# Performance work log

Hardware: AMD Instinct MI355X
Metric: run time of the kernel (lower is better)

## Reference

```python
import jax, jax.numpy as jnp
import numpy as np

D_MODEL = 512
NUM_HEADS = 8
HEAD_DIM = D_MODEL // NUM_HEADS
MAX_REL = 2


def setup_inputs() -> dict:
    key = jax.random.key(0)
    ks = jax.random.split(key, 12)
    B, S = 2, 4096
    std = 1.0 / np.sqrt(D_MODEL)
    inp = {
        'q': jax.random.normal(ks[0], (B, S, D_MODEL), jnp.float32),
        'k': jax.random.normal(ks[1], (B, S, D_MODEL), jnp.float32),
        'v': jax.random.normal(ks[2], (B, S, D_MODEL), jnp.float32),
        'Wq': jax.random.normal(ks[3], (D_MODEL, D_MODEL), jnp.float32) * std,
        'bq': jnp.zeros((D_MODEL,), jnp.float32),
        'Wk': jax.random.normal(ks[4], (D_MODEL, D_MODEL), jnp.float32) * std,
        'bk': jnp.zeros((D_MODEL,), jnp.float32),
        'Wv': jax.random.normal(ks[5], (D_MODEL, D_MODEL), jnp.float32) * std,
        'bv': jnp.zeros((D_MODEL,), jnp.float32),
        'Wo': jax.random.normal(ks[6], (D_MODEL, D_MODEL), jnp.float32) * std,
        'bo': jnp.zeros((D_MODEL,), jnp.float32),
        'rel_pos': jax.random.normal(ks[7], (NUM_HEADS, 2 * MAX_REL + 1), jnp.float32),
    }
    return inp


def _rel_bias(rel_pos, seq_len):
    pos = jnp.arange(seq_len)
    rel = pos[None, :] - pos[:, None]              # [S,S]
    idx = jnp.clip(rel, -MAX_REL, MAX_REL) + MAX_REL
    return rel_pos[:, idx]                         # [H,S,S]


def reference(q, k, v, Wq, bq, Wk, bk, Wv, bv, Wo, bo, rel_pos):
    B, S, D = q.shape
    H, Hd = NUM_HEADS, HEAD_DIM
    # torch Linear: x @ W.T + b
    Q = (q @ Wq.T + bq).reshape(B, S, H, Hd).transpose(0, 2, 1, 3)  # [B,H,S,Hd]
    K = (k @ Wk.T + bk).reshape(B, S, H, Hd).transpose(0, 2, 1, 3)
    V = (v @ Wv.T + bv).reshape(B, S, H, Hd).transpose(0, 2, 1, 3)
    scores = jnp.einsum('bhqd,bhkd->bhqk', Q, K) / jnp.sqrt(jnp.float32(Hd))
    scores = scores + _rel_bias(rel_pos, S)[None]                  # [B,H,S,S]
    probs = jax.nn.softmax(scores, axis=-1)
    attn = jnp.einsum('bhqk,bhkd->bhqd', probs, V)                 # [B,H,S,Hd]
    attn = attn.transpose(0, 2, 1, 3).reshape(B, S, D)
    return attn @ Wo.T + bo
```

## Files before the change

kernel.cpp:

```cpp
#include <hip/hip_runtime.h>

typedef __bf16 bf16_t;
typedef __bf16 bf16x4 __attribute__((ext_vector_type(4)));
typedef __bf16 bf16x8 __attribute__((ext_vector_type(8)));
typedef float f32x4 __attribute__((ext_vector_type(4)));

#define MFMA16(a, b, c) __builtin_amdgcn_mfma_f32_16x16x32_bf16(a, b, c, 0, 0, 0)
#define LOG2E 1.4426950408889634f

#define GLL(g, l)                                                      \
  __builtin_amdgcn_global_load_lds(                                    \
      (const __attribute__((address_space(1))) void*)(g),              \
      (__attribute__((address_space(3))) void*)(l), 16, 0, 0)

static constexpr int NB = 2;
static constexpr int SEQ = 4096;
static constexpr int DM = 512;
static constexpr int NH = 8;
static constexpr int HD = 64;
static constexpr int M_ROWS = NB * SEQ;

__global__ __launch_bounds__(256) void cvt_w_kernel(
    const float* __restrict__ w0, const float* __restrict__ w1,
    const float* __restrict__ w2, const float* __restrict__ w3,
    bf16_t* __restrict__ out) {
  const float* src = (blockIdx.y == 0) ? w0 : (blockIdx.y == 1) ? w1
                   : (blockIdx.y == 2) ? w2 : w3;
  int i = (blockIdx.x * 256 + threadIdx.x) * 4;
  float4 v = *(const float4*)(src + i);
  bf16_t* o = out + blockIdx.y * (DM * DM) + i;
  o[0] = (bf16_t)v.x; o[1] = (bf16_t)v.y; o[2] = (bf16_t)v.z; o[3] = (bf16_t)v.w;
}

template <int XMODE, int TM>
__device__ __forceinline__ void gemm_body(
    const void* __restrict__ Xv, const bf16_t* __restrict__ Wm,
    const float* __restrict__ bias, void* __restrict__ Out,
    int omode, float scale) {
  constexpr int MB = TM / 32;
  __shared__ bf16_t Asm[TM * 32];
  __shared__ bf16_t Bsm[128 * 32];

  const int tid = threadIdx.x;
  const int w = tid >> 6;
  const int lane = tid & 63;
  const int quad = lane >> 4, l15 = lane & 15;
  const int m0 = blockIdx.x * TM;
  const int n0 = blockIdx.y * 128;
  const int moff = (w & 1) * (TM / 2);
  const int noff = (w >> 1) * 64;

  const float* Xf = (const float*)Xv;
  const bf16_t* Xb = (const bf16_t*)Xv;

  f32x4 acc[MB][4];
#pragma unroll
  for (int mb = 0; mb < MB; mb++)
#pragma unroll
    for (int nb = 0; nb < 4; nb++) { acc[mb][nb][0] = 0.f; acc[mb][nb][1] = 0.f; acc[mb][nb][2] = 0.f; acc[mb][nb][3] = 0.f; }

  for (int k0 = 0; k0 < DM; k0 += 32) {
    __syncthreads();
#pragma unroll
    for (int j = 0; j < 2; j++) {
      const int c = w * 64 + lane + j * 256;
      GLL(Wm + (size_t)(n0 + (c >> 2)) * DM + k0 + (c & 3) * 8,
          Bsm + (w * 64 + j * 256) * 8);
    }
    if (XMODE == 1) {
#pragma unroll
      for (int j = 0; j < TM * 32 / 2048; j++) {
        const int c = w * 64 + lane + j * 256;
        GLL(Xb + (size_t)(m0 + (c >> 2)) * DM + k0 + (c & 3) * 8,
            Asm + (w * 64 + j * 256) * 8);
      }
    } else {
      const int arow = tid >> 1;
      const int aseg = (tid & 1) * 16;
      const float* src = Xf + (size_t)(m0 + arow) * DM + k0 + aseg;
      float4 x0 = *(const float4*)(src);
      float4 x1 = *(const float4*)(src + 4);
      float4 x2 = *(const float4*)(src + 8);
      float4 x3 = *(const float4*)(src + 12);
      bf16x8 p0, p1;
      p0[0] = (bf16_t)x0.x; p0[1] = (bf16_t)x0.y; p0[2] = (bf16_t)x0.z; p0[3] = (bf16_t)x0.w;
      p0[4] = (bf16_t)x1.x; p0[5] = (bf16_t)x1.y; p0[6] = (bf16_t)x1.z; p0[7] = (bf16_t)x1.w;
      p1[0] = (bf16_t)x2.x; p1[1] = (bf16_t)x2.y; p1[2] = (bf16_t)x2.z; p1[3] = (bf16_t)x2.w;
      p1[4] = (bf16_t)x3.x; p1[5] = (bf16_t)x3.y; p1[6] = (bf16_t)x3.z; p1[7] = (bf16_t)x3.w;
      *(bf16x8*)&Asm[arow * 32 + aseg] = p0;
      *(bf16x8*)&Asm[arow * 32 + aseg + 8] = p1;
    }
    __syncthreads();

    bf16x8 bfr[4];
#pragma unroll
    for (int nb = 0; nb < 4; nb++)
      bfr[nb] = *(const bf16x8*)&Bsm[(noff + nb * 16 + l15) * 32 + 8 * quad];
#pragma unroll
    for (int mb = 0; mb < MB; mb++) {
      bf16x8 a = *(const bf16x8*)&Asm[(moff + mb * 16 + l15) * 32 + 8 * quad];
#pragma unroll
      for (int nb = 0; nb < 4; nb++) acc[mb][nb] = MFMA16(a, bfr[nb], acc[mb][nb]);
    }
  }

#pragma unroll
  for (int nb = 0; nb < 4; nb++) {
    const int n = n0 + noff + nb * 16 + l15;
    const float bn = bias[n];
    const int h = n >> 6, dd = n & 63;
#pragma unroll
    for (int mb = 0; mb < MB; mb++) {
      const int mbase = m0 + moff + mb * 16 + quad * 4;
      const int bb = mbase >> 12, s = mbase & 4095;
      if (omode == 0) {
#pragma unroll
        for (int r = 0; r < 4; r++) {
          const float val = (acc[mb][nb][r] + bn) * scale;
          ((bf16_t*)Out)[(size_t)((bb * NH + h) * SEQ + s + r) * HD + dd] = (bf16_t)val;
        }
      } else if (omode == 1) {
        bf16x4 pk;
#pragma unroll
        for (int r = 0; r < 4; r++) pk[r] = (bf16_t)(acc[mb][nb][r] + bn);
        *(bf16x4*)&((bf16_t*)Out)[(((size_t)(bb * NH + h) * HD + dd) << 12) + s] = pk;
      } else {
#pragma unroll
        for (int r = 0; r < 4; r++)
          ((float*)Out)[(size_t)(mbase + r) * DM + n] = acc[mb][nb][r] + bn;
      }
    }
  }
}

__global__ __launch_bounds__(256, 3) void qkv_kernel(
    const float* __restrict__ q, const float* __restrict__ k,
    const float* __restrict__ v, const bf16_t* __restrict__ Wall,
    const float* __restrict__ bq, const float* __restrict__ bk,
    const float* __restrict__ bv, bf16_t* __restrict__ Qb,
    bf16_t* __restrict__ Kb, bf16_t* __restrict__ Vb, float qscale) {
  const int z = blockIdx.z;
  const float* X = (z == 0) ? q : (z == 1) ? k : v;
  const float* bias = (z == 0) ? bq : (z == 1) ? bk : bv;
  bf16_t* Out = (z == 0) ? Qb : (z == 1) ? Kb : Vb;
  gemm_body<0, 128>(X, Wall + (size_t)z * DM * DM, bias, Out,
                    (z == 2) ? 1 : 0, (z == 0) ? qscale : 1.0f);
}

__global__ __launch_bounds__(256, 3) void oproj_kernel(
    const bf16_t* __restrict__ X, const bf16_t* __restrict__ Wm,
    const float* __restrict__ bias, float* __restrict__ Out) {
  gemm_body<1, 64>(X, Wm, bias, Out, 2, 1.0f);
}

__global__ __launch_bounds__(256, 2) void attn_kernel(
    const bf16_t* __restrict__ Qb, const bf16_t* __restrict__ Kb,
    const bf16_t* __restrict__ Vb, const float* __restrict__ rel_pos,
    bf16_t* __restrict__ attn_out) {
  __shared__ bf16_t Kt[64 * 64];
  __shared__ bf16_t Vt[64 * 64];
  __shared__ bf16_t Pt[4][32 * 72];

  const int w = threadIdx.x >> 6;
  const int lane = threadIdx.x & 63;
  const int quad = lane >> 4, l15 = lane & 15;
  const int bh = blockIdx.y;
  const int b = bh >> 3, h = bh & 7;
  const int qlo = blockIdx.x * 128 + w * 32;

  const float rb0 = rel_pos[h * 5 + 0] * LOG2E;
  const float rb1 = rel_pos[h * 5 + 1] * LOG2E;
  const float rb2 = rel_pos[h * 5 + 2] * LOG2E;
  const float rb3 = rel_pos[h * 5 + 3] * LOG2E;
  const float rb4 = rel_pos[h * 5 + 4] * LOG2E;

  bf16x8 qf[2][2];
#pragma unroll
  for (int mb = 0; mb < 2; mb++)
#pragma unroll
    for (int kd = 0; kd < 2; kd++)
      qf[mb][kd] = *(const bf16x8*)(Qb + (size_t)(bh * SEQ + qlo + mb * 16 + l15) * HD + kd * 32 + 8 * quad);

  f32x4 o[2][4];
#pragma unroll
  for (int mb = 0; mb < 2; mb++)
#pragma unroll
    for (int db = 0; db < 4; db++) { o[mb][db][0] = 0.f; o[mb][db][1] = 0.f; o[mb][db][2] = 0.f; o[mb][db][3] = 0.f; }
  f32x4 l4[2];
  l4[0][0] = 0.f; l4[0][1] = 0.f; l4[0][2] = 0.f; l4[0][3] = 0.f;
  l4[1][0] = 0.f; l4[1][1] = 0.f; l4[1][2] = 0.f; l4[1][3] = 0.f;

  bf16x8 ones;
#pragma unroll
  for (int i = 0; i < 8; i++) ones[i] = (bf16_t)1.0f;

  const int srow = (w << 4) + (lane >> 3);
  const int scol = (((lane & 7) ^ (lane >> 3)) << 3);
  const bf16_t* kg0 = Kb + ((size_t)(bh * SEQ + srow) << 6) + scol;
  const bf16_t* kg1 = kg0 + (8 << 6);
  const bf16_t* vg0 = Vb + ((size_t)(bh * HD + srow) << 12) + scol;
  const bf16_t* vg1 = vg0 + (8 << 12);
  bf16_t* kl0 = Kt + (w << 10);
  bf16_t* kl1 = kl0 + 512;
  bf16_t* vl0 = Vt + (w << 10);
  bf16_t* vl1 = vl0 + 512;

  const int swz = l15 & 7;
  const bf16_t* kf0 = Kt + (l15 << 6) + (((quad    ) ^ swz) << 3);
  const bf16_t* kf1 = Kt + (l15 << 6) + (((quad + 4) ^ swz) << 3);
  const bf16_t* vf0 = Vt + (l15 << 6) + (((quad    ) ^ swz) << 3);
  const bf16_t* vf1 = Vt + (l15 << 6) + (((quad + 4) ^ swz) << 3);

  for (int t = 0; t < 64; t++) {
    const int kk0 = t * 64;
    __syncthreads();
    GLL(kg0 + (t << 12), kl0);
    GLL(kg1 + (t << 12), kl1);
    GLL(vg0 + (t << 6), vl0);
    GLL(vg1 + (t << 6), vl1);
    __syncthreads();

    float cini;
    bool nearband = false;
    if (kk0 >= qlo + 33) {
      cini = rb4 - 16.0f;
    } else if (kk0 + 63 <= qlo - 2) {
      cini = rb0 - 16.0f;
    } else {
      cini = -16.0f;
      nearband = true;
    }

    f32x4 s[2][4];
#pragma unroll
    for (int mb = 0; mb < 2; mb++)
#pragma unroll
      for (int kb = 0; kb < 4; kb++) { s[mb][kb][0] = cini; s[mb][kb][1] = cini; s[mb][kb][2] = cini; s[mb][kb][3] = cini; }
#pragma unroll
    for (int kb = 0; kb < 4; kb++) {
      bf16x8 kA0 = *(const bf16x8*)(kf0 + (kb << 10));
      bf16x8 kA1 = *(const bf16x8*)(kf1 + (kb << 10));
      s[0][kb] = MFMA16(kA0, qf[0][0], s[0][kb]);
      s[0][kb] = MFMA16(kA1, qf[0][1], s[0][kb]);
      s[1][kb] = MFMA16(kA0, qf[1][0], s[1][kb]);
      s[1][kb] = MFMA16(kA1, qf[1][1], s[1][kb]);
    }

    if (nearband) {
#pragma unroll
      for (int mb = 0; mb < 2; mb++) {
        const int qg = qlo + mb * 16 + l15;
#pragma unroll
        for (int kb = 0; kb < 4; kb++)
#pragma unroll
          for (int r = 0; r < 4; r++) {
            int dl = kk0 + kb * 16 + quad * 4 + r - qg;
            float bias = dl <= -2 ? rb0
                       : (dl >= 2 ? rb4
                       : (dl == -1 ? rb1 : (dl == 0 ? rb2 : rb3)));
            s[mb][kb][r] += bias;
          }
      }
    }

#pragma unroll
    for (int mb = 0; mb < 2; mb++) {
      bf16_t* Pr = &Pt[w][(mb * 16 + l15) * 72];
#pragma unroll
      for (int kb = 0; kb < 4; kb++) {
        bf16x4 pk;
#pragma unroll
        for (int r = 0; r < 4; r++)
          pk[r] = (bf16_t)__builtin_amdgcn_exp2f(s[mb][kb][r]);
        *(bf16x4*)&Pr[kb * 16 + quad * 4] = pk;
      }
    }

    bf16x8 pf[2][2];
#pragma unroll
    for (int mb = 0; mb < 2; mb++)
#pragma unroll
      for (int kc = 0; kc < 2; kc++)
        pf[mb][kc] = *(const bf16x8*)&Pt[w][(mb * 16 + l15) * 72 + kc * 32 + quad * 8];

    l4[0] = MFMA16(ones, pf[0][0], l4[0]);
    l4[0] = MFMA16(ones, pf[0][1], l4[0]);
    l4[1] = MFMA16(ones, pf[1][0], l4[1]);
    l4[1] = MFMA16(ones, pf[1][1], l4[1]);

#pragma unroll
    for (int db = 0; db < 4; db++) {
      bf16x8 vA0 = *(const bf16x8*)(vf0 + (db << 10));
      bf16x8 vA1 = *(const bf16x8*)(vf1 + (db << 10));
      o[0][db] = MFMA16(vA0, pf[0][0], o[0][db]);
      o[0][db] = MFMA16(vA1, pf[0][1], o[0][db]);
      o[1][db] = MFMA16(vA0, pf[1][0], o[1][db]);
      o[1][db] = MFMA16(vA1, pf[1][1], o[1][db]);
    }
  }

#pragma unroll
  for (int mb = 0; mb < 2; mb++) {
    const float inv = 1.0f / l4[mb][0];
    const int qg = qlo + mb * 16 + l15;
#pragma unroll
    for (int db = 0; db < 4; db++) {
      bf16x4 pk;
#pragma unroll
      for (int r = 0; r < 4; r++) pk[r] = (bf16_t)(o[mb][db][r] * inv);
      *(bf16x4*)(attn_out + (size_t)(b * SEQ + qg) * DM + h * HD + db * 16 + quad * 4) = pk;
    }
  }
}

extern "C" void kernel_launch(void* const* d_in, const int* in_sizes, int n_in,
                              void* d_out, int out_size, void* d_ws, size_t ws_size,
                              hipStream_t stream) {
  const float* q   = (const float*)d_in[0];
  const float* k   = (const float*)d_in[1];
  const float* v   = (const float*)d_in[2];
  const float* Wq  = (const float*)d_in[3];
  const float* bq  = (const float*)d_in[4];
  const float* Wk  = (const float*)d_in[5];
  const float* bk  = (const float*)d_in[6];
  const float* Wv  = (const float*)d_in[7];
  const float* bv  = (const float*)d_in[8];
  const float* Wo  = (const float*)d_in[9];
  const float* bo  = (const float*)d_in[10];
  const float* rel = (const float*)d_in[11];

  char* ws = (char*)d_ws;
  bf16_t* Wbf  = (bf16_t*)ws;
  bf16_t* Qbuf = (bf16_t*)(ws + (size_t)(2  << 20));
  bf16_t* Kbuf = (bf16_t*)(ws + (size_t)(10 << 20));
  bf16_t* Vbuf = (bf16_t*)(ws + (size_t)(18 << 20));
  bf16_t* Abuf = (bf16_t*)(ws + (size_t)(26 << 20));

  cvt_w_kernel<<<dim3(256, 4), 256, 0, stream>>>(Wq, Wk, Wv, Wo, Wbf);

  const float qscale = LOG2E / 8.0f;
  qkv_kernel<<<dim3(64, 4, 3), 256, 0, stream>>>(
      q, k, v, Wbf, bq, bk, bv, Qbuf, Kbuf, Vbuf, qscale);

  attn_kernel<<<dim3(32, 16), 256, 0, stream>>>(Qbuf, Kbuf, Vbuf, rel, Abuf);

  oproj_kernel<<<dim3(128, 4), 256, 0, stream>>>(Abuf, Wbf + 3 * DM * DM, bo, (float*)d_out);
}
```

Measured before the change: 241.3 us.

## Split attention keys across waves with LDS reduction; widen GEMM K-step to 64

The attention kernel now has each block own 64 queries, and each of its four waves handles a different 32-key slice. K and V fragments are loaded straight from global memory into registers, so the shared-memory staging and the per-iteration block barriers go away. Partial outputs and row sums are combined at the end through an LDS tree reduction, and the grid doubles to keep the block count up. The projection GEMMs switch to 64-wide K tiles with XOR-swizzled LDS to halve barrier count and avoid bank conflicts, at the cost of more LDS and uncoalesced direct global fragment loads in attention.

```diff
diff --git a/kernel.cpp b/kernel.cpp
--- a/kernel.cpp
+++ b/kernel.cpp
@@ -7,6 +7,7 @@
 
 #define MFMA16(a, b, c) __builtin_amdgcn_mfma_f32_16x16x32_bf16(a, b, c, 0, 0, 0)
 #define LOG2E 1.4426950408889634f
+#define SHIFT 16.0f
 
 #define GLL(g, l)                                                      \
   __builtin_amdgcn_global_load_lds(                                    \
@@ -38,69 +39,70 @@
     const float* __restrict__ bias, void* __restrict__ Out,
     int omode, float scale) {
   constexpr int MB = TM / 32;
-  __shared__ bf16_t Asm[TM * 32];
-  __shared__ bf16_t Bsm[128 * 32];
+  __shared__ bf16_t Asm[TM * 64];
+  __shared__ bf16_t Bsm[128 * 64];
 
   const int tid = threadIdx.x;
   const int w = tid >> 6;
   const int lane = tid & 63;
   const int quad = lane >> 4, l15 = lane & 15;
+  const int l8 = lane >> 3;
+  const int swcol = ((lane & 7) ^ l8) * 8;
   const int m0 = blockIdx.x * TM;
   const int n0 = blockIdx.y * 128;
   const int moff = (w & 1) * (TM / 2);
   const int noff = (w >> 1) * 64;
 
-  const float* Xf = (const float*)Xv;
-  const bf16_t* Xb = (const bf16_t*)Xv;
-
   f32x4 acc[MB][4];
 #pragma unroll
   for (int mb = 0; mb < MB; mb++)
 #pragma unroll
     for (int nb = 0; nb < 4; nb++) { acc[mb][nb][0] = 0.f; acc[mb][nb][1] = 0.f; acc[mb][nb][2] = 0.f; acc[mb][nb][3] = 0.f; }
 
-  for (int k0 = 0; k0 < DM; k0 += 32) {
+  for (int k0 = 0; k0 < DM; k0 += 64) {
     __syncthreads();
 #pragma unroll
-    for (int j = 0; j < 2; j++) {
-      const int c = w * 64 + lane + j * 256;
-      GLL(Wm + (size_t)(n0 + (c >> 2)) * DM + k0 + (c & 3) * 8,
-          Bsm + (w * 64 + j * 256) * 8);
+    for (int j = 0; j < 4; j++) {
+      const int row = j * 32 + w * 8 + l8;
+      GLL(Wm + (size_t)(n0 + row) * DM + k0 + swcol, Bsm + (j * 256 + w * 64) * 8);
     }
     if (XMODE == 1) {
 #pragma unroll
-      for (int j = 0; j < TM * 32 / 2048; j++) {
-        const int c = w * 64 + lane + j * 256;
-        GLL(Xb + (size_t)(m0 + (c >> 2)) * DM + k0 + (c & 3) * 8,
-            Asm + (w * 64 + j * 256) * 8);
+      for (int j = 0; j < TM / 32; j++) {
+        const int row = j * 32 + w * 8 + l8;
+        GLL((const bf16_t*)Xv + (size_t)(m0 + row) * DM + k0 + swcol,
+            Asm + (j * 256 + w * 64) * 8);
       }
     } else {
       const int arow = tid >> 1;
-      const int aseg = (tid & 1) * 16;
-      const float* src = Xf + (size_t)(m0 + arow) * DM + k0 + aseg;
-      float4 x0 = *(const float4*)(src);
-      float4 x1 = *(const float4*)(src + 4);
-      float4 x2 = *(const float4*)(src + 8);
-      float4 x3 = *(const float4*)(src + 12);
-      bf16x8 p0, p1;
-      p0[0] = (bf16_t)x0.x; p0[1] = (bf16_t)x0.y; p0[2] = (bf16_t)x0.z; p0[3] = (bf16_t)x0.w;
-      p0[4] = (bf16_t)x1.x; p0[5] = (bf16_t)x1.y; p0[6] = (bf16_t)x1.z; p0[7] = (bf16_t)x1.w;
-      p1[0] = (bf16_t)x2.x; p1[1] = (bf16_t)x2.y; p1[2] = (bf16_t)x2.z; p1[3] = (bf16_t)x2.w;
-      p1[4] = (bf16_t)x3.x; p1[5] = (bf16_t)x3.y; p1[6] = (bf16_t)x3.z; p1[7] = (bf16_t)x3.w;
-      *(bf16x8*)&Asm[arow * 32 + aseg] = p0;
-      *(bf16x8*)&Asm[arow * 32 + aseg + 8] = p1;
+      const int ahalf = (tid & 1) * 32;
+      const float* src = (const float*)Xv + (size_t)(m0 + arow) * DM + k0 + ahalf;
+      const int chb = (tid & 1) * 4;
+#pragma unroll
+      for (int i = 0; i < 4; i++) {
+        float4 lo = *(const float4*)(src + i * 8);
+        float4 hi = *(const float4*)(src + i * 8 + 4);
+        bf16x8 pk;
+        pk[0] = (bf16_t)lo.x; pk[1] = (bf16_t)lo.y; pk[2] = (bf16_t)lo.z; pk[3] = (bf16_t)lo.w;
+        pk[4] = (bf16_t)hi.x; pk[5] = (bf16_t)hi.y; pk[6] = (bf16_t)hi.z; pk[7] = (bf16_t)hi.w;
+        *(bf16x8*)&Asm[arow * 64 + (((chb + i) ^ (arow & 7)) * 8)] = pk;
+      }
     }
     __syncthreads();
 
-    bf16x8 bfr[4];
-#pragma unroll
-    for (int nb = 0; nb < 4; nb++)
-      bfr[nb] = *(const bf16x8*)&Bsm[(noff + nb * 16 + l15) * 32 + 8 * quad];
-#pragma unroll
-    for (int mb = 0; mb < MB; mb++) {
-      bf16x8 a = *(const bf16x8*)&Asm[(moff + mb * 16 + l15) * 32 + 8 * quad];
-#pragma unroll
-      for (int nb = 0; nb < 4; nb++) acc[mb][nb] = MFMA16(a, bfr[nb], acc[mb][nb]);
+#pragma unroll
+    for (int kd = 0; kd < 2; kd++) {
+      const int fch = ((kd * 4 + quad) ^ (l15 & 7)) * 8;
+      bf16x8 bfr[4];
+#pragma unroll
+      for (int nb = 0; nb < 4; nb++)
+        bfr[nb] = *(const bf16x8*)&Bsm[(noff + nb * 16 + l15) * 64 + fch];
+#pragma unroll
+      for (int mb = 0; mb < MB; mb++) {
+        bf16x8 a = *(const bf16x8*)&Asm[(moff + mb * 16 + l15) * 64 + fch];
+#pragma unroll
+        for (int nb = 0; nb < 4; nb++) acc[mb][nb] = MFMA16(a, bfr[nb], acc[mb][nb]);
+      }
     }
   }
 
@@ -157,16 +159,19 @@
     const bf16_t* __restrict__ Qb, const bf16_t* __restrict__ Kb,
     const bf16_t* __restrict__ Vb, const float* __restrict__ rel_pos,
     bf16_t* __restrict__ attn_out) {
-  __shared__ bf16_t Kt[64 * 64];
-  __shared__ bf16_t Vt[64 * 64];
-  __shared__ bf16_t Pt[4][32 * 72];
-
-  const int w = threadIdx.x >> 6;
-  const int lane = threadIdx.x & 63;
+  __shared__ char smem[34816];
+  const int tid = threadIdx.x;
+  const int w = tid >> 6;
+  const int lane = tid & 63;
   const int quad = lane >> 4, l15 = lane & 15;
   const int bh = blockIdx.y;
   const int b = bh >> 3, h = bh & 7;
-  const int qlo = blockIdx.x * 128 + w * 32;
+  const int qlo = blockIdx.x * 64;
+
+  bf16_t* Pw = (bf16_t*)smem + w * (64 * 40);
+  float* redA = (float*)smem;
+  float* redB = redA + 4096;
+  float* redL = redB + 4096;
 
   const float rb0 = rel_pos[h * 5 + 0] * LOG2E;
   const float rb1 = rel_pos[h * 5 + 1] * LOG2E;
@@ -174,141 +179,178 @@
   const float rb3 = rel_pos[h * 5 + 3] * LOG2E;
   const float rb4 = rel_pos[h * 5 + 4] * LOG2E;
 
-  bf16x8 qf[2][2];
-#pragma unroll
-  for (int mb = 0; mb < 2; mb++)
+  bf16x8 qf[4][2];
+#pragma unroll
+  for (int qb = 0; qb < 4; qb++)
 #pragma unroll
     for (int kd = 0; kd < 2; kd++)
-      qf[mb][kd] = *(const bf16x8*)(Qb + (size_t)(bh * SEQ + qlo + mb * 16 + l15) * HD + kd * 32 + 8 * quad);
-
-  f32x4 o[2][4];
-#pragma unroll
-  for (int mb = 0; mb < 2; mb++)
-#pragma unroll
-    for (int db = 0; db < 4; db++) { o[mb][db][0] = 0.f; o[mb][db][1] = 0.f; o[mb][db][2] = 0.f; o[mb][db][3] = 0.f; }
-  f32x4 l4[2];
-  l4[0][0] = 0.f; l4[0][1] = 0.f; l4[0][2] = 0.f; l4[0][3] = 0.f;
-  l4[1][0] = 0.f; l4[1][1] = 0.f; l4[1][2] = 0.f; l4[1][3] = 0.f;
+      qf[qb][kd] = *(const bf16x8*)(Qb + (size_t)(bh * SEQ + qlo + qb * 16 + l15) * HD + kd * 32 + 8 * quad);
+
+  f32x4 o[4][4];
+#pragma unroll
+  for (int db = 0; db < 4; db++)
+#pragma unroll
+    for (int qb = 0; qb < 4; qb++) { o[db][qb][0] = 0.f; o[db][qb][1] = 0.f; o[db][qb][2] = 0.f; o[db][qb][3] = 0.f; }
+  f32x4 l4[4];
+#pragma unroll
+  for (int qb = 0; qb < 4; qb++) { l4[qb][0] = 0.f; l4[qb][1] = 0.f; l4[qb][2] = 0.f; l4[qb][3] = 0.f; }
 
   bf16x8 ones;
 #pragma unroll
   for (int i = 0; i < 8; i++) ones[i] = (bf16_t)1.0f;
 
-  const int srow = (w << 4) + (lane >> 3);
-  const int scol = (((lane & 7) ^ (lane >> 3)) << 3);
-  const bf16_t* kg0 = Kb + ((size_t)(bh * SEQ + srow) << 6) + scol;
-  const bf16_t* kg1 = kg0 + (8 << 6);
-  const bf16_t* vg0 = Vb + ((size_t)(bh * HD + srow) << 12) + scol;
-  const bf16_t* vg1 = vg0 + (8 << 12);
-  bf16_t* kl0 = Kt + (w << 10);
-  bf16_t* kl1 = kl0 + 512;
-  bf16_t* vl0 = Vt + (w << 10);
-  bf16_t* vl1 = vl0 + 512;
-
-  const int swz = l15 & 7;
-  const bf16_t* kf0 = Kt + (l15 << 6) + (((quad    ) ^ swz) << 3);
-  const bf16_t* kf1 = Kt + (l15 << 6) + (((quad + 4) ^ swz) << 3);
-  const bf16_t* vf0 = Vt + (l15 << 6) + (((quad    ) ^ swz) << 3);
-  const bf16_t* vf1 = Vt + (l15 << 6) + (((quad + 4) ^ swz) << 3);
-
-  for (int t = 0; t < 64; t++) {
-    const int kk0 = t * 64;
-    __syncthreads();
-    GLL(kg0 + (t << 12), kl0);
-    GLL(kg1 + (t << 12), kl1);
-    GLL(vg0 + (t << 6), vl0);
-    GLL(vg1 + (t << 6), vl1);
-    __syncthreads();
+  const bf16_t* Kbase = Kb + (size_t)bh * SEQ * HD;
+  const bf16_t* Vbase = Vb + (((size_t)bh * HD) << 12);
+
+  for (int t = 0; t < 32; t++) {
+    const int kk0 = t * 128 + w * 32;
+
+    bf16x8 kA[2][2];
+#pragma unroll
+    for (int kkb = 0; kkb < 2; kkb++)
+#pragma unroll
+      for (int kd = 0; kd < 2; kd++)
+        kA[kkb][kd] = *(const bf16x8*)(Kbase + (size_t)(kk0 + kkb * 16 + l15) * HD + kd * 32 + quad * 8);
+    bf16x8 vA[4];
+#pragma unroll
+    for (int db = 0; db < 4; db++)
+      vA[db] = *(const bf16x8*)(Vbase + (((size_t)(db * 16 + l15)) << 12) + kk0 + quad * 8);
 
     float cini;
     bool nearband = false;
-    if (kk0 >= qlo + 33) {
-      cini = rb4 - 16.0f;
-    } else if (kk0 + 63 <= qlo - 2) {
-      cini = rb0 - 16.0f;
+    if (kk0 >= qlo + 65) {
+      cini = rb4 - SHIFT;
+    } else if (kk0 + 33 <= qlo) {
+      cini = rb0 - SHIFT;
     } else {
-      cini = -16.0f;
+      cini = -SHIFT;
       nearband = true;
     }
 
     f32x4 s[2][4];
 #pragma unroll
-    for (int mb = 0; mb < 2; mb++)
-#pragma unroll
-      for (int kb = 0; kb < 4; kb++) { s[mb][kb][0] = cini; s[mb][kb][1] = cini; s[mb][kb][2] = cini; s[mb][kb][3] = cini; }
-#pragma unroll
-    for (int kb = 0; kb < 4; kb++) {
-      bf16x8 kA0 = *(const bf16x8*)(kf0 + (kb << 10));
-      bf16x8 kA1 = *(const bf16x8*)(kf1 + (kb << 10));
-      s[0][kb] = MFMA16(kA0, qf[0][0], s[0][kb]);
-      s[0][kb] = MFMA16(kA1, qf[0][1], s[0][kb]);
-      s[1][kb] = MFMA16(kA0, qf[1][0], s[1][kb]);
-      s[1][kb] = MFMA16(kA1, qf[1][1], s[1][kb]);
-    }
+    for (int kkb = 0; kkb < 2; kkb++)
+#pragma unroll
+      for (int qb = 0; qb < 4; qb++) { s[kkb][qb][0] = cini; s[kkb][qb][1] = cini; s[kkb][qb][2] = cini; s[kkb][qb][3] = cini; }
+#pragma unroll
+    for (int kkb = 0; kkb < 2; kkb++)
+#pragma unroll
+      for (int qb = 0; qb < 4; qb++) {
+        s[kkb][qb] = MFMA16(kA[kkb][0], qf[qb][0], s[kkb][qb]);
+        s[kkb][qb] = MFMA16(kA[kkb][1], qf[qb][1], s[kkb][qb]);
+      }
 
     if (nearband) {
 #pragma unroll
-      for (int mb = 0; mb < 2; mb++) {
-        const int qg = qlo + mb * 16 + l15;
-#pragma unroll
-        for (int kb = 0; kb < 4; kb++)
+      for (int kkb = 0; kkb < 2; kkb++)
+#pragma unroll
+        for (int qb = 0; qb < 4; qb++) {
+          const int qg = qlo + qb * 16 + l15;
 #pragma unroll
           for (int r = 0; r < 4; r++) {
-            int dl = kk0 + kb * 16 + quad * 4 + r - qg;
+            int dl = kk0 + kkb * 16 + quad * 4 + r - qg;
             float bias = dl <= -2 ? rb0
                        : (dl >= 2 ? rb4
                        : (dl == -1 ? rb1 : (dl == 0 ? rb2 : rb3)));
-            s[mb][kb][r] += bias;
+            s[kkb][qb][r] += bias;
           }
-      }
-    }
-
-#pragma unroll
-    for (int mb = 0; mb < 2; mb++) {
-      bf16_t* Pr = &Pt[w][(mb * 16 + l15) * 72];
-#pragma unroll
-      for (int kb = 0; kb < 4; kb++) {
+        }
+    }
+
+#pragma unroll
+    for (int qb = 0; qb < 4; qb++) {
+      bf16_t* Pr = &Pw[(qb * 16 + l15) * 40];
+#pragma unroll
+      for (int kkb = 0; kkb < 2; kkb++) {
         bf16x4 pk;
 #pragma unroll
         for (int r = 0; r < 4; r++)
-          pk[r] = (bf16_t)__builtin_amdgcn_exp2f(s[mb][kb][r]);
-        *(bf16x4*)&Pr[kb * 16 + quad * 4] = pk;
-      }
-    }
-
-    bf16x8 pf[2][2];
-#pragma unroll
-    for (int mb = 0; mb < 2; mb++)
-#pragma unroll
-      for (int kc = 0; kc < 2; kc++)
-        pf[mb][kc] = *(const bf16x8*)&Pt[w][(mb * 16 + l15) * 72 + kc * 32 + quad * 8];
-
-    l4[0] = MFMA16(ones, pf[0][0], l4[0]);
-    l4[0] = MFMA16(ones, pf[0][1], l4[0]);
-    l4[1] = MFMA16(ones, pf[1][0], l4[1]);
-    l4[1] = MFMA16(ones, pf[1][1], l4[1]);
-
-#pragma unroll
-    for (int db = 0; db < 4; db++) {
-      bf16x8 vA0 = *(const bf16x8*)(vf0 + (db << 10));
-      bf16x8 vA1 = *(const bf16x8*)(vf1 + (db << 10));
-      o[0][db] = MFMA16(vA0, pf[0][0], o[0][db]);
-      o[0][db] = MFMA16(vA1, pf[0][1], o[0][db]);
-      o[1][db] = MFMA16(vA0, pf[1][0], o[1][db]);
-      o[1][db] = MFMA16(vA1, pf[1][1], o[1][db]);
-    }
-  }
-
-#pragma unroll
-  for (int mb = 0; mb < 2; mb++) {
-    const float inv = 1.0f / l4[mb][0];
-    const int qg = qlo + mb * 16 + l15;
-#pragma unroll
-    for (int db = 0; db < 4; db++) {
-      bf16x4 pk;
-#pragma unroll
-      for (int r = 0; r < 4; r++) pk[r] = (bf16_t)(o[mb][db][r] * inv);
-      *(bf16x4*)(attn_out + (size_t)(b * SEQ + qg) * DM + h * HD + db * 16 + quad * 4) = pk;
+          pk[r] = (bf16_t)__builtin_amdgcn_exp2f(s[kkb][qb][r]);
+        *(bf16x4*)&Pr[kkb * 16 + quad * 4] = pk;
+      }
+    }
+
+    bf16x8 pf[4];
+#pragma unroll
+    for (int qb = 0; qb < 4; qb++)
+      pf[qb] = *(const bf16x8*)&Pw[(qb * 16 + l15) * 40 + quad * 8];
+#pragma unroll
+    for (int qb = 0; qb < 4; qb++) l4[qb] = MFMA16(ones, pf[qb], l4[qb]);
+#pragma unroll
+    for (int db = 0; db < 4; db++)
+#pragma unroll
+      for (int qb = 0; qb < 4; qb++)
+        o[db][qb] = MFMA16(vA[db], pf[qb], o[db][qb]);
+  }
+
+  __syncthreads();
+  if (w == 2) {
+#pragma unroll
+    for (int db = 0; db < 4; db++)
+#pragma unroll
+      for (int qb = 0; qb < 4; qb++)
+        *(f32x4*)&redA[((db * 4 + qb) * 64 + lane) * 4] = o[db][qb];
+  }
+  if (w == 3) {
+#pragma unroll
+    for (int db = 0; db < 4; db++)
+#pragma unroll
+      for (int qb = 0; qb < 4; qb++)
+        *(f32x4*)&redB[((db * 4 + qb) * 64 + lane) * 4] = o[db][qb];
+  }
+  if (quad == 0) {
+#pragma unroll
+    for (int qb = 0; qb < 4; qb++) redL[w * 64 + qb * 16 + l15] = l4[qb][0];
+  }
+  __syncthreads();
+  if (w == 0) {
+#pragma unroll
+    for (int db = 0; db < 4; db++)
+#pragma unroll
+      for (int qb = 0; qb < 4; qb++) {
+        f32x4 tv = *(const f32x4*)&redA[((db * 4 + qb) * 64 + lane) * 4];
+        o[db][qb][0] += tv[0]; o[db][qb][1] += tv[1]; o[db][qb][2] += tv[2]; o[db][qb][3] += tv[3];
+      }
+  }
+  if (w == 1) {
+#pragma unroll
+    for (int db = 0; db < 4; db++)
+#pragma unroll
+      for (int qb = 0; qb < 4; qb++) {
+        f32x4 tv = *(const f32x4*)&redB[((db * 4 + qb) * 64 + lane) * 4];
+        o[db][qb][0] += tv[0]; o[db][qb][1] += tv[1]; o[db][qb][2] += tv[2]; o[db][qb][3] += tv[3];
+      }
+  }
+  __syncthreads();
+  if (w == 1) {
+#pragma unroll
+    for (int db = 0; db < 4; db++)
+#pragma unroll
+      for (int qb = 0; qb < 4; qb++)
+        *(f32x4*)&redA[((db * 4 + qb) * 64 + lane) * 4] = o[db][qb];
+  }
+  __syncthreads();
+  if (w == 0) {
+#pragma unroll
+    for (int db = 0; db < 4; db++)
+#pragma unroll
+      for (int qb = 0; qb < 4; qb++) {
+        f32x4 tv = *(const f32x4*)&redA[((db * 4 + qb) * 64 + lane) * 4];
+        o[db][qb][0] += tv[0]; o[db][qb][1] += tv[1]; o[db][qb][2] += tv[2]; o[db][qb][3] += tv[3];
+      }
+#pragma unroll
+    for (int qb = 0; qb < 4; qb++) {
+      const int q16 = qb * 16 + l15;
+      const float lt = redL[q16] + redL[64 + q16] + redL[128 + q16] + redL[192 + q16];
+      const float inv = 1.0f / lt;
+      const int qg = qlo + q16;
+#pragma unroll
+      for (int db = 0; db < 4; db++) {
+        bf16x4 pk;
+#pragma unroll
+        for (int r = 0; r < 4; r++) pk[r] = (bf16_t)(o[db][qb][r] * inv);
+        *(bf16x4*)(attn_out + (size_t)(b * SEQ + qg) * DM + h * HD + db * 16 + quad * 4) = pk;
+      }
     }
   }
 }
@@ -342,7 +384,7 @@
   qkv_kernel<<<dim3(64, 4, 3), 256, 0, stream>>>(
       q, k, v, Wbf, bq, bk, bv, Qbuf, Kbuf, Vbuf, qscale);
 
-  attn_kernel<<<dim3(32, 16), 256, 0, stream>>>(Qbuf, Kbuf, Vbuf, rel, Abuf);
+  attn_kernel<<<dim3(64, 16), 256, 0, stream>>>(Qbuf, Kbuf, Vbuf, rel, Abuf);
 
   oproj_kernel<<<dim3(128, 4), 256, 0, stream>>>(Abuf, Wbf + 3 * DM * DM, bo, (float*)d_out);
 }
```

Result: slower. 275.4 us (+14.1%).
